# Kernel optimization log

Measured on AMD Instinct MI355X. Metric: run time of the kernel, lower is better.

The kernel has to match this reference:

```python
import jax, jax.numpy as jnp
import numpy as np

K = 2            # top-k experts
TEMPERATURE = 1.0
EPS = 1e-9


def setup_inputs() -> dict:
    key = jax.random.key(0)
    k1, k2 = jax.random.split(key)
    B, S, D = 4, 4096, 4096
    G, E = 4, 64
    x = jax.random.normal(k1, (B, S, D), dtype=jnp.float32)
    # stacked gate weights, one [E, D] Linear weight per gate head
    W = jax.random.normal(k2, (G, E, D), dtype=jnp.float32) * 0.02
    return {"x": x, "W": W}


def reference(x, W):
    # per-head logits over experts: [B, S, G, E]; jitter disabled (eval / jitter_noise=0)
    logits = jnp.einsum('bsd,ged->bsge', x, W) * (1.0 / TEMPERATURE)
    probs = jax.nn.softmax(logits, axis=-1)          # softmax per head
    probs_full = probs.mean(axis=2)                  # consensus over heads: [B, S, E]
    topk_vals, idx = jax.lax.top_k(probs_full, K)    # sorted descending, matches aten.topk
    den = jnp.sum(topk_vals, axis=-1, keepdims=True)
    scores = topk_vals / jnp.maximum(den, EPS)       # clamp_min(den, 1e-9)
    pf = jax.lax.stop_gradient(probs_full)           # aux stats under no_grad
    importance = pf.mean(axis=(0, 1))                # [E]
    load = (pf > 0.0).astype(pf.dtype).mean(axis=(0, 1))  # [E]
    return idx, scores, probs_full, importance, load
```

## Files before the change

### kernel.cpp

```cpp
#include <hip/hip_runtime.h>

typedef _Float16 f16x8  __attribute__((ext_vector_type(8)));
typedef float    f32x4  __attribute__((ext_vector_type(4)));
typedef float    f32x16 __attribute__((ext_vector_type(16)));

#define MROWS 16384
#define NCOLS 256
#define KDIM  4096
#define BM    128
#define BK    32
#define LDA   34

#define OUT_SCORES 32768
#define OUT_PF     65536
#define OUT_IMP    1114112
#define OUT_LOAD   1114176

#define FIN_BLOCKS 1024

__global__ __launch_bounds__(256) void wprep(const float* __restrict__ W,
                                             _Float16* __restrict__ wfHi,
                                             _Float16* __restrict__ wfLo) {
    int t  = blockIdx.x * 256 + threadIdx.x;
    int n  = t >> 9;
    int k8 = t & 511;
    const float* src = W + ((size_t)n * KDIM + (size_t)k8 * 8);
    f16x8 hi, lo;
#pragma unroll
    for (int j = 0; j < 8; ++j) {
        float x = src[j];
        _Float16 h = (_Float16)x;
        hi[j] = h;
        lo[j] = (_Float16)(x - (float)h);
    }
    int NT    = n >> 5;
    int ksg   = k8 >> 2;
    int ksub  = (k8 >> 1) & 1;
    int lane  = (n & 31) + ((k8 & 1) << 5);
    size_t dst = ((size_t)((ksg * 8 + NT) * 2 + ksub) * 64 + (size_t)lane) * 8;
    *(f16x8*)(wfHi + dst) = hi;
    *(f16x8*)(wfLo + dst) = lo;
}

__global__ __launch_bounds__(512, 4) void gemm3(const float* __restrict__ X,
        const _Float16* __restrict__ wfHi, const _Float16* __restrict__ wfLo,
        float* __restrict__ lsplit, int kQ) {
    __shared__ _Float16 aHi[2][BM * LDA];
    __shared__ _Float16 aLo[2][BM * LDA];

    const int tid  = threadIdx.x;
    const int lane = tid & 63;
    const int w    = tid >> 6;
    const int wr   = w >> 2;
    const int wc   = w & 3;
    const int mt   = blockIdx.x & 127;
    const int s    = blockIdx.x >> 7;
    const int m0   = mt * BM;
    const int k0   = s * kQ;
    const int iters = kQ / BK;

    f32x16 acc[2][2];
#pragma unroll
    for (int a = 0; a < 2; ++a)
#pragma unroll
        for (int b = 0; b < 2; ++b)
#pragma unroll
            for (int q = 0; q < 16; ++q) acc[a][b][q] = 0.f;

    const int sr = tid >> 2;
    const int sq = tid & 3;
    const float* xrow = X + ((size_t)(m0 + sr) * KDIM + (size_t)k0 + sq * 8);
    const int woff = sr * LDA + sq * 8;

    const int roff = (wr * 64 + (lane & 31)) * LDA + (lane >> 5) * 8;

    const size_t bbase = (size_t)(k0 >> 5) * 8192 + (size_t)(2 * wc) * 1024 + (size_t)lane * 8;
    const _Float16* BH = wfHi + bbase;
    const _Float16* BL = wfLo + bbase;

    f32x4 xq0 = *(const f32x4*)(xrow);
    f32x4 xq1 = *(const f32x4*)(xrow + 4);

    for (int i = 0; i < iters; ++i) {
        f32x4 xn0, xn1;
        {
            const float* xp = xrow + (size_t)((i + 1 < iters) ? (i + 1) : 0) * BK;
            xn0 = *(const f32x4*)(xp);
            xn1 = *(const f32x4*)(xp + 4);
        }

        float xv[8];
        xv[0] = xq0[0]; xv[1] = xq0[1]; xv[2] = xq0[2]; xv[3] = xq0[3];
        xv[4] = xq1[0]; xv[5] = xq1[1]; xv[6] = xq1[2]; xv[7] = xq1[3];
        f16x8 h, l;
#pragma unroll
        for (int j = 0; j < 8; ++j) {
            _Float16 ha = (_Float16)xv[j];
            h[j] = ha;
            l[j] = (_Float16)(xv[j] - (float)ha);
        }

        *(f16x8*)(&aHi[i & 1][woff]) = h;
        *(f16x8*)(&aLo[i & 1][woff]) = l;

        asm volatile("s_waitcnt lgkmcnt(0)" ::: "memory");
        __builtin_amdgcn_s_barrier();
        __builtin_amdgcn_sched_barrier(0);

        f16x8 bH[2][2], bL[2][2];
#pragma unroll
        for (int ni = 0; ni < 2; ++ni)
#pragma unroll
            for (int ks = 0; ks < 2; ++ks) {
                size_t off = (size_t)i * 8192 + (size_t)ni * 1024 + (size_t)ks * 512;
                bH[ni][ks] = *(const f16x8*)(BH + off);
                bL[ni][ks] = *(const f16x8*)(BL + off);
            }

        const _Float16* rAH = &aHi[i & 1][roff];
        const _Float16* rAL = &aLo[i & 1][roff];
        __builtin_amdgcn_s_setprio(1);
#pragma unroll
        for (int mi = 0; mi < 2; ++mi) {
            f16x8 aH0 = *(const f16x8*)(rAH + mi * 32 * LDA);
            f16x8 aH1 = *(const f16x8*)(rAH + mi * 32 * LDA + 16);
            f16x8 aL0 = *(const f16x8*)(rAL + mi * 32 * LDA);
            f16x8 aL1 = *(const f16x8*)(rAL + mi * 32 * LDA + 16);
#pragma unroll
            for (int ni = 0; ni < 2; ++ni) {
                acc[mi][ni] = __builtin_amdgcn_mfma_f32_32x32x16_f16(aH0, bH[ni][0], acc[mi][ni], 0, 0, 0);
                acc[mi][ni] = __builtin_amdgcn_mfma_f32_32x32x16_f16(aH1, bH[ni][1], acc[mi][ni], 0, 0, 0);
                acc[mi][ni] = __builtin_amdgcn_mfma_f32_32x32x16_f16(aH0, bL[ni][0], acc[mi][ni], 0, 0, 0);
                acc[mi][ni] = __builtin_amdgcn_mfma_f32_32x32x16_f16(aH1, bL[ni][1], acc[mi][ni], 0, 0, 0);
                acc[mi][ni] = __builtin_amdgcn_mfma_f32_32x32x16_f16(aL0, bH[ni][0], acc[mi][ni], 0, 0, 0);
                acc[mi][ni] = __builtin_amdgcn_mfma_f32_32x32x16_f16(aL1, bH[ni][1], acc[mi][ni], 0, 0, 0);
            }
        }
        __builtin_amdgcn_s_setprio(0);

        xq0 = xn0; xq1 = xn1;
    }

    float* outp = lsplit + (size_t)s * ((size_t)MROWS * NCOLS);
#pragma unroll
    for (int mi = 0; mi < 2; ++mi) {
#pragma unroll
        for (int ni = 0; ni < 2; ++ni) {
            int col   = wc * 64 + ni * 32 + (lane & 31);
            int rbase = m0 + wr * 64 + mi * 32 + ((lane >> 5) << 2);
#pragma unroll
            for (int reg = 0; reg < 16; ++reg) {
                int row = rbase + (reg & 3) + ((reg >> 2) << 3);
                outp[(size_t)row * NCOLS + col] = acc[mi][ni][reg];
            }
        }
    }
}

__global__ __launch_bounds__(256) void finalize(const float* __restrict__ lsplit,
                                                int nsplit, float* __restrict__ out,
                                                float* __restrict__ paux) {
    __shared__ float sImp[64], sLoad[64];
    const int tid = threadIdx.x;
    if (tid < 64) { sImp[tid] = 0.f; sLoad[tid] = 0.f; }
    __syncthreads();

    const int i   = tid & 15;
    const int grp = tid >> 4;
    const int r   = blockIdx.x * 16 + grp;

    float v[16];
#pragma unroll
    for (int t = 0; t < 16; ++t) {
        size_t off = (size_t)r * 256 + (size_t)i + 16 * t;
        float a = lsplit[off];
        for (int s = 1; s < nsplit; ++s)
            a += lsplit[(size_t)s * ((size_t)MROWS * NCOLS) + off];
        v[t] = a;
    }

    float hm[4];
#pragma unroll
    for (int g = 0; g < 4; ++g) {
        float m = fmaxf(fmaxf(v[4*g], v[4*g+1]), fmaxf(v[4*g+2], v[4*g+3]));
#pragma unroll
        for (int msk = 1; msk < 16; msk <<= 1)
            m = fmaxf(m, __shfl_xor(m, msk));
        hm[g] = m;
    }
    float p[16], inv[4];
#pragma unroll
    for (int g = 0; g < 4; ++g) {
        float sa = 0.f;
#pragma unroll
        for (int q = 0; q < 4; ++q) { p[4*g+q] = __expf(v[4*g+q] - hm[g]); sa += p[4*g+q]; }
#pragma unroll
        for (int msk = 1; msk < 16; msk <<= 1)
            sa += __shfl_xor(sa, msk);
        inv[g] = 1.f / sa;
    }

    float pf[4];
#pragma unroll
    for (int et = 0; et < 4; ++et) {
        pf[et] = 0.25f * (p[et] * inv[0] + p[4+et] * inv[1] + p[8+et] * inv[2] + p[12+et] * inv[3]);
        out[OUT_PF + (size_t)r * 64 + i + 16 * et] = pf[et];
        atomicAdd(&sImp[i + 16 * et], pf[et]);
        atomicAdd(&sLoad[i + 16 * et], pf[et] > 0.f ? 1.f : 0.f);
    }

    float v1 = -3.4e38f, v2 = -3.4e38f; int e1 = 0, e2 = 0;
#pragma unroll
    for (int et = 0; et < 4; ++et) {
        int e = i + 16 * et; float val = pf[et];
        if (val > v1) { v2 = v1; e2 = e1; v1 = val; e1 = e; }
        else if (val > v2) { v2 = val; e2 = e; }
    }
#pragma unroll
    for (int msk = 1; msk < 16; msk <<= 1) {
        float o1 = __shfl_xor(v1, msk); int oe1 = __shfl_xor(e1, msk);
        float o2 = __shfl_xor(v2, msk); int oe2 = __shfl_xor(e2, msk);
        bool ob = (o1 > v1) || (o1 == v1 && oe1 < e1);
        if (ob) {
            bool vb = (v1 > o2) || (v1 == o2 && e1 < oe2);
            v2 = vb ? v1 : o2; e2 = vb ? e1 : oe2;
            v1 = o1; e1 = oe1;
        } else {
            bool nb = (o1 > v2) || (o1 == v2 && oe1 < e2);
            v2 = nb ? o1 : v2; e2 = nb ? oe1 : e2;
        }
    }
    if (i == 0) {
        float den = fmaxf(v1 + v2, 1e-9f);
        out[(size_t)r * 2]              = (float)e1;
        out[(size_t)r * 2 + 1]          = (float)e2;
        out[OUT_SCORES + (size_t)r * 2]     = v1 / den;
        out[OUT_SCORES + (size_t)r * 2 + 1] = v2 / den;
    }
    __syncthreads();
    if (tid < 128)
        paux[(size_t)blockIdx.x * 128 + tid] = (tid < 64) ? sImp[tid] : sLoad[tid - 64];
}

__global__ __launch_bounds__(1024) void reduce_aux(const float* __restrict__ paux,
                                                   float* __restrict__ out) {
    __shared__ float part[8][128];
    const int t = threadIdx.x & 127;
    const int g = threadIdx.x >> 7;
    float s = 0.f;
    for (int b = g * 128; b < g * 128 + 128; ++b)
        s += paux[(size_t)b * 128 + t];
    part[g][t] = s;
    __syncthreads();
    if (threadIdx.x < 128) {
        float a = 0.f;
#pragma unroll
        for (int g2 = 0; g2 < 8; ++g2) a += part[g2][t];
        out[OUT_IMP + t] = a * (1.0f / 16384.0f);
    }
}

extern "C" void kernel_launch(void* const* d_in, const int* in_sizes, int n_in,
                              void* d_out, int out_size, void* d_ws, size_t ws_size,
                              hipStream_t stream) {
    const float* X = (const float*)d_in[0];
    const float* W = (const float*)d_in[1];
    float* out = (float*)d_out;
    char* ws = (char*)d_ws;

    _Float16* wfHi = (_Float16*)ws;
    _Float16* wfLo = (_Float16*)(ws + (2u << 20));
    float* lsplit  = (float*)(ws + (4u << 20));

    const size_t per = 16u << 20;
    int nsplit = (ws_size >= (4u << 20) + 4 * per + (1u << 20)) ? 4
               : (ws_size >= (4u << 20) + 2 * per + (1u << 20)) ? 2 : 1;

    float* paux = (float*)(ws + (4u << 20) + (size_t)nsplit * per);

    wprep<<<512, 256, 0, stream>>>(W, wfHi, wfLo);
    gemm3<<<128 * nsplit, 512, 0, stream>>>(X, wfHi, wfLo, lsplit, KDIM / nsplit);
    finalize<<<FIN_BLOCKS, 256, 0, stream>>>(lsplit, nsplit, out, paux);
    reduce_aux<<<1, 1024, 0, stream>>>(paux, out);
}
```

Measured before the change: 498.9 us.

## Prefetch X four K-steps ahead and double-buffer B fragments in registers

The GEMM main loop now loads 128 K-columns of X into registers at once, one outer step ahead. It also double-buffers the W fragments in registers, so the next step's global loads are issued before the current MFMAs run. The aim is to hide global load latency better. In exchange, register pressure rises, so launch bounds drop from 4 to 2 blocks per SM, and the K-split is reduced from 4 to 2, halving partial-sum traffic but also the grid size.

Result: no change. 491.3 us (-1.5%).

```diff
diff --git a/kernel.cpp b/kernel.cpp
--- a/kernel.cpp
+++ b/kernel.cpp
@@ -9,6 +9,7 @@
 #define KDIM  4096
 #define BM    128
 #define BK    32
+#define BKO   128
 #define LDA   34
 
 #define OUT_SCORES 32768
@@ -42,7 +43,7 @@
     *(f16x8*)(wfLo + dst) = lo;
 }
 
-__global__ __launch_bounds__(512, 4) void gemm3(const float* __restrict__ X,
+__global__ __launch_bounds__(512, 2) void gemm3(const float* __restrict__ X,
         const _Float16* __restrict__ wfHi, const _Float16* __restrict__ wfLo,
         float* __restrict__ lsplit, int kQ) {
     __shared__ _Float16 aHi[2][BM * LDA];
@@ -57,7 +58,7 @@
     const int s    = blockIdx.x >> 7;
     const int m0   = mt * BM;
     const int k0   = s * kQ;
-    const int iters = kQ / BK;
+    const int outers = kQ >> 7;
 
     f32x16 acc[2][2];
 #pragma unroll
@@ -65,80 +66,96 @@
 #pragma unroll
         for (int b = 0; b < 2; ++b)
 #pragma unroll
-            for (int q = 0; q < 16; ++q) acc[a][b][q] = 0.f;
-
-    const int sr = tid >> 2;
-    const int sq = tid & 3;
-    const float* xrow = X + ((size_t)(m0 + sr) * KDIM + (size_t)k0 + sq * 8);
-    const int woff = sr * LDA + sq * 8;
+            for (int qq = 0; qq < 16; ++qq) acc[a][b][qq] = 0.f;
+
+    const int rr = tid >> 2;
+    const int q  = tid & 3;
+    const float* xbase = X + ((size_t)(m0 + rr) * KDIM + (size_t)k0 + (size_t)q * 8);
+    const int woff = rr * LDA + q * 8;
 
     const int roff = (wr * 64 + (lane & 31)) * LDA + (lane >> 5) * 8;
 
     const size_t bbase = (size_t)(k0 >> 5) * 8192 + (size_t)(2 * wc) * 1024 + (size_t)lane * 8;
-    const _Float16* BH = wfHi + bbase;
-    const _Float16* BL = wfLo + bbase;
-
-    f32x4 xq0 = *(const f32x4*)(xrow);
-    f32x4 xq1 = *(const f32x4*)(xrow + 4);
-
-    for (int i = 0; i < iters; ++i) {
-        f32x4 xn0, xn1;
-        {
-            const float* xp = xrow + (size_t)((i + 1 < iters) ? (i + 1) : 0) * BK;
-            xn0 = *(const f32x4*)(xp);
-            xn1 = *(const f32x4*)(xp + 4);
+    const _Float16* pBH = wfHi + bbase;
+    const _Float16* pBL = wfLo + bbase;
+
+    f32x4 xs[8];
+#pragma unroll
+    for (int jh = 0; jh < 8; ++jh)
+        xs[jh] = *(const f32x4*)(xbase + (jh >> 1) * 32 + (jh & 1) * 4);
+
+    f16x8 bH[2][2][2], bL[2][2][2];
+#pragma unroll
+    for (int ni = 0; ni < 2; ++ni)
+#pragma unroll
+        for (int ks = 0; ks < 2; ++ks) {
+            bH[0][ni][ks] = *(const f16x8*)(pBH + ni * 1024 + ks * 512);
+            bL[0][ni][ks] = *(const f16x8*)(pBL + ni * 1024 + ks * 512);
         }
 
-        float xv[8];
-        xv[0] = xq0[0]; xv[1] = xq0[1]; xv[2] = xq0[2]; xv[3] = xq0[3];
-        xv[4] = xq1[0]; xv[5] = xq1[1]; xv[6] = xq1[2]; xv[7] = xq1[3];
-        f16x8 h, l;
-#pragma unroll
-        for (int j = 0; j < 8; ++j) {
-            _Float16 ha = (_Float16)xv[j];
-            h[j] = ha;
-            l[j] = (_Float16)(xv[j] - (float)ha);
+    for (int o = 0; o < outers; ++o) {
+#pragma unroll
+        for (int j = 0; j < 4; ++j) {
+            float xv[8];
+            xv[0] = xs[2*j][0]; xv[1] = xs[2*j][1]; xv[2] = xs[2*j][2]; xv[3] = xs[2*j][3];
+            xv[4] = xs[2*j+1][0]; xv[5] = xs[2*j+1][1]; xv[6] = xs[2*j+1][2]; xv[7] = xs[2*j+1][3];
+            f16x8 h, l;
+#pragma unroll
+            for (int e = 0; e < 8; ++e) {
+                _Float16 ha = (_Float16)xv[e];
+                h[e] = ha;
+                l[e] = (_Float16)(xv[e] - (float)ha);
+            }
+
+            if (j == 3) {
+                const float* xp = xbase + (size_t)((o + 1 < outers) ? (o + 1) : 0) * BKO;
+#pragma unroll
+                for (int jh = 0; jh < 8; ++jh)
+                    xs[jh] = *(const f32x4*)(xp + (jh >> 1) * 32 + (jh & 1) * 4);
+            }
+
+            *(f16x8*)(&aHi[j & 1][woff]) = h;
+            *(f16x8*)(&aLo[j & 1][woff]) = l;
+
+            asm volatile("s_waitcnt lgkmcnt(0)" ::: "memory");
+            __builtin_amdgcn_s_barrier();
+            __builtin_amdgcn_sched_barrier(0);
+
+            {
+                bool lastInner = (o == outers - 1) && (j == 3);
+                const _Float16* nBH = lastInner ? (wfHi + bbase) : (pBH + 8192);
+                const _Float16* nBL = lastInner ? (wfLo + bbase) : (pBL + 8192);
+#pragma unroll
+                for (int ni = 0; ni < 2; ++ni)
+#pragma unroll
+                    for (int ks = 0; ks < 2; ++ks) {
+                        bH[(j + 1) & 1][ni][ks] = *(const f16x8*)(nBH + ni * 1024 + ks * 512);
+                        bL[(j + 1) & 1][ni][ks] = *(const f16x8*)(nBL + ni * 1024 + ks * 512);
+                    }
+                pBH = nBH; pBL = nBL;
+            }
+
+            const _Float16* rAH = &aHi[j & 1][roff];
+            const _Float16* rAL = &aLo[j & 1][roff];
+            __builtin_amdgcn_s_setprio(1);
+#pragma unroll
+            for (int mi = 0; mi < 2; ++mi) {
+                f16x8 aH0 = *(const f16x8*)(rAH + mi * 32 * LDA);
+                f16x8 aH1 = *(const f16x8*)(rAH + mi * 32 * LDA + 16);
+                f16x8 aL0 = *(const f16x8*)(rAL + mi * 32 * LDA);
+                f16x8 aL1 = *(const f16x8*)(rAL + mi * 32 * LDA + 16);
+#pragma unroll
+                for (int ni = 0; ni < 2; ++ni) {
+                    acc[mi][ni] = __builtin_amdgcn_mfma_f32_32x32x16_f16(aH0, bH[j & 1][ni][0], acc[mi][ni], 0, 0, 0);
+                    acc[mi][ni] = __builtin_amdgcn_mfma_f32_32x32x16_f16(aH1, bH[j & 1][ni][1], acc[mi][ni], 0, 0, 0);
+                    acc[mi][ni] = __builtin_amdgcn_mfma_f32_32x32x16_f16(aH0, bL[j & 1][ni][0], acc[mi][ni], 0, 0, 0);
+                    acc[mi][ni] = __builtin_amdgcn_mfma_f32_32x32x16_f16(aH1, bL[j & 1][ni][1], acc[mi][ni], 0, 0, 0);
+                    acc[mi][ni] = __builtin_amdgcn_mfma_f32_32x32x16_f16(aL0, bH[j & 1][ni][0], acc[mi][ni], 0, 0, 0);
+                    acc[mi][ni] = __builtin_amdgcn_mfma_f32_32x32x16_f16(aL1, bH[j & 1][ni][1], acc[mi][ni], 0, 0, 0);
+                }
+            }
+            __builtin_amdgcn_s_setprio(0);
         }
-
-        *(f16x8*)(&aHi[i & 1][woff]) = h;
-        *(f16x8*)(&aLo[i & 1][woff]) = l;
-
-        asm volatile("s_waitcnt lgkmcnt(0)" ::: "memory");
-        __builtin_amdgcn_s_barrier();
-        __builtin_amdgcn_sched_barrier(0);
-
-        f16x8 bH[2][2], bL[2][2];
-#pragma unroll
-        for (int ni = 0; ni < 2; ++ni)
-#pragma unroll
-            for (int ks = 0; ks < 2; ++ks) {
-                size_t off = (size_t)i * 8192 + (size_t)ni * 1024 + (size_t)ks * 512;
-                bH[ni][ks] = *(const f16x8*)(BH + off);
-                bL[ni][ks] = *(const f16x8*)(BL + off);
-            }
-
-        const _Float16* rAH = &aHi[i & 1][roff];
-        const _Float16* rAL = &aLo[i & 1][roff];
-        __builtin_amdgcn_s_setprio(1);
-#pragma unroll
-        for (int mi = 0; mi < 2; ++mi) {
-            f16x8 aH0 = *(const f16x8*)(rAH + mi * 32 * LDA);
-            f16x8 aH1 = *(const f16x8*)(rAH + mi * 32 * LDA + 16);
-            f16x8 aL0 = *(const f16x8*)(rAL + mi * 32 * LDA);
-            f16x8 aL1 = *(const f16x8*)(rAL + mi * 32 * LDA + 16);
-#pragma unroll
-            for (int ni = 0; ni < 2; ++ni) {
-                acc[mi][ni] = __builtin_amdgcn_mfma_f32_32x32x16_f16(aH0, bH[ni][0], acc[mi][ni], 0, 0, 0);
-                acc[mi][ni] = __builtin_amdgcn_mfma_f32_32x32x16_f16(aH1, bH[ni][1], acc[mi][ni], 0, 0, 0);
-                acc[mi][ni] = __builtin_amdgcn_mfma_f32_32x32x16_f16(aH0, bL[ni][0], acc[mi][ni], 0, 0, 0);
-                acc[mi][ni] = __builtin_amdgcn_mfma_f32_32x32x16_f16(aH1, bL[ni][1], acc[mi][ni], 0, 0, 0);
-                acc[mi][ni] = __builtin_amdgcn_mfma_f32_32x32x16_f16(aL0, bH[ni][0], acc[mi][ni], 0, 0, 0);
-                acc[mi][ni] = __builtin_amdgcn_mfma_f32_32x32x16_f16(aL1, bH[ni][1], acc[mi][ni], 0, 0, 0);
-            }
-        }
-        __builtin_amdgcn_s_setprio(0);
-
-        xq0 = xn0; xq1 = xn1;
     }
 
     float* outp = lsplit + (size_t)s * ((size_t)MROWS * NCOLS);
@@ -193,7 +210,7 @@
     for (int g = 0; g < 4; ++g) {
         float sa = 0.f;
 #pragma unroll
-        for (int q = 0; q < 4; ++q) { p[4*g+q] = __expf(v[4*g+q] - hm[g]); sa += p[4*g+q]; }
+        for (int qq = 0; qq < 4; ++qq) { p[4*g+qq] = __expf(v[4*g+qq] - hm[g]); sa += p[4*g+qq]; }
 #pragma unroll
         for (int msk = 1; msk < 16; msk <<= 1)
             sa += __shfl_xor(sa, msk);
@@ -273,8 +290,7 @@
     float* lsplit  = (float*)(ws + (4u << 20));
 
     const size_t per = 16u << 20;
-    int nsplit = (ws_size >= (4u << 20) + 4 * per + (1u << 20)) ? 4
-               : (ws_size >= (4u << 20) + 2 * per + (1u << 20)) ? 2 : 1;
+    int nsplit = (ws_size >= (4u << 20) + 2 * per + (1u << 20)) ? 2 : 1;
 
     float* paux = (float*)(ws + (4u << 20) + (size_t)nsplit * per);
 
```
